# Kernel optimization log

Hardware: AMD Instinct MI355X
Metric: run time of the kernel (lower is better)

The kernel has to match this reference:

```python
import jax, jax.numpy as jnp
import numpy as np

B, S, P, D, H = 2, 4096, 1024, 1024, 16  # batch, byte seq, patches, d_model, heads


def setup_inputs() -> dict:
    key = jax.random.key(0)
    ks = jax.random.split(key, 8)
    init = 0.02
    queries = jax.random.normal(ks[0], (B, S, D), dtype=jnp.float32)
    patch_representations = jax.random.normal(ks[1], (B, P, D), dtype=jnp.float32)
    patch_boundaries = jax.random.randint(ks[2], (B, S), 0, 2, dtype=jnp.int32)
    wq = jax.random.normal(ks[3], (D, D), dtype=jnp.float32) * init
    wk = jax.random.normal(ks[4], (D, D), dtype=jnp.float32) * init
    wv = jax.random.normal(ks[5], (D, D), dtype=jnp.float32) * init
    wo = jax.random.normal(ks[6], (D, D), dtype=jnp.float32) * init
    bq = jnp.zeros((D,), jnp.float32)
    bk = jnp.zeros((D,), jnp.float32)
    bv = jnp.zeros((D,), jnp.float32)
    bo = jnp.zeros((D,), jnp.float32)
    return {"queries": queries, "patch_representations": patch_representations,
            "patch_boundaries": patch_boundaries,
            "wq": wq, "wk": wk, "wv": wv, "wo": wo,
            "bq": bq, "bk": bk, "bv": bv, "bo": bo}


def reference(queries, patch_representations, patch_boundaries,
              wq, wk, wv, wo, bq, bk, bv, bo):
    b, s, d = queries.shape
    p = patch_representations.shape[1]
    h = H
    dh = d // h
    scale = 1.0 / jnp.sqrt(jnp.asarray(dh, queries.dtype))

    # in-projections (torch Linear: x @ W.T + b)
    q = (queries @ wq.T + bq).reshape(b, s, h, dh)
    k = (patch_representations @ wk.T + bk).reshape(b, p, h, dh)
    v = (patch_representations @ wv.T + bv).reshape(b, p, h, dh)

    # scores: [b, h, s, p]
    scores = jnp.einsum('bqhd,bkhd->bhqk', q, k) * scale

    # data-dependent patch-boundary mask: byte t may attend to patch j iff j <= cumsum(boundaries)[t]
    patch_idx = jnp.cumsum(patch_boundaries, axis=1)          # [b, s]
    mask = jnp.arange(p)[None, None, :] > patch_idx[:, :, None]  # [b, s, p], True = masked
    scores = jnp.where(mask[:, None, :, :], jnp.finfo(scores.dtype).min, scores)

    attn = jax.nn.softmax(scores, axis=-1)                    # dropout inactive (eval)
    out = jnp.einsum('bhqk,bkhd->bqhd', attn, v).reshape(b, s, d)
    return out @ wo.T + bo
```

## Files before the change

### kernel.cpp

```cpp
#include <hip/hip_runtime.h>


#define B_ 2
#define S_ 4096
#define P_ 1024
#define D_ 1024
#define H_ 16
#define DH_ 64

#define NCONV 14336

typedef __attribute__((ext_vector_type(8))) short short8;
typedef __attribute__((ext_vector_type(4))) float f32x4;

#define KSCALE 0.18033688011112042f

#if __has_builtin(__builtin_amdgcn_exp2f)
#define EXP2(x) __builtin_amdgcn_exp2f(x)
#else
#define EXP2(x) exp2f(x)
#endif

static __device__ __forceinline__ unsigned short f2bf(float f) {
    unsigned int u = __float_as_uint(f);
    u += 0x7FFFu + ((u >> 16) & 1u);
    return (unsigned short)(u >> 16);
}

static __device__ __forceinline__ void gll16(const unsigned short* g,
                                             const unsigned short* l) {
    __builtin_amdgcn_global_load_lds(
        (const __attribute__((address_space(1))) unsigned int*)g,
        (__attribute__((address_space(3))) unsigned int*)l,
        16, 0, 0);
}

__global__ __launch_bounds__(256) void xattn_convert_all(
    const float* __restrict__ queries, const float* __restrict__ patches,
    const float* __restrict__ wq, const float* __restrict__ wk,
    const float* __restrict__ wv, const float* __restrict__ wo,
    unsigned short* __restrict__ qb, unsigned short* __restrict__ pb,
    unsigned short* __restrict__ wqb, unsigned short* __restrict__ wkb,
    unsigned short* __restrict__ wvb, unsigned short* __restrict__ wob,
    const int* __restrict__ bounds, int* __restrict__ pidx) {
    if (blockIdx.x >= NCONV) {
        __shared__ int sdata[256];
        int b = blockIdx.x - NCONV;
        int t = threadIdx.x;
        const int* src = bounds + b * S_ + t * 16;
        int vals[16];
        int run = 0;
#pragma unroll
        for (int i = 0; i < 16; ++i) { run += src[i]; vals[i] = run; }
        sdata[t] = run;
        __syncthreads();
        for (int off = 1; off < 256; off <<= 1) {
            int v = (t >= off) ? sdata[t - off] : 0;
            __syncthreads();
            sdata[t] += v;
            __syncthreads();
        }
        int prefix = (t > 0) ? sdata[t - 1] : 0;
        int* dst = pidx + b * S_ + t * 16;
#pragma unroll
        for (int i = 0; i < 16; ++i) dst[i] = prefix + vals[i];
        return;
    }
    const int NQ = (B_ * S_ * D_) / 4;
    const int NP = (B_ * P_ * D_) / 4;
    const int NW = (D_ * D_) / 4;
    int i = blockIdx.x * 256 + threadIdx.x;
    const float* src;
    unsigned short* dst;
    int j;
    if (i < NQ) { src = queries; dst = qb; j = i; }
    else if (i < NQ + NP) { src = patches; dst = pb; j = i - NQ; }
    else {
        int k = i - NQ - NP;
        int wsel = k >> 18;
        j = k & (NW - 1);
        if (wsel == 0) { src = wq; dst = wqb; }
        else if (wsel == 1) { src = wk; dst = wkb; }
        else if (wsel == 2) { src = wv; dst = wvb; }
        else { src = wo; dst = wob; }
    }
    float4 v = ((const float4*)src)[j];
    ushort4 o;
    o.x = f2bf(v.x); o.y = f2bf(v.y); o.z = f2bf(v.z); o.w = f2bf(v.w);
    ((ushort4*)dst)[j] = o;
}

__global__ __launch_bounds__(256) void xattn_gemm_qkv(
    const unsigned short* __restrict__ qb, const unsigned short* __restrict__ pb,
    const unsigned short* __restrict__ wqb, const unsigned short* __restrict__ wkb,
    const unsigned short* __restrict__ wvb,
    const float* __restrict__ bq, const float* __restrict__ bk,
    const float* __restrict__ bv,
    unsigned short* __restrict__ Qout, unsigned short* __restrict__ Kout,
    unsigned short* __restrict__ Vout) {
    const int K = 1024, N = 1024;
    const int byy = blockIdx.y;
    int z, my;
    if (byy < 64)      { z = 0; my = byy; }
    else if (byy < 80) { z = 1; my = byy - 64; }
    else               { z = 2; my = byy - 80; }
    const unsigned short* A = (z == 0) ? qb : pb;
    const unsigned short* W = (z == 0) ? wqb : ((z == 1) ? wkb : wvb);
    const float* bias = (z == 0) ? bq : ((z == 1) ? bk : bv);

    __shared__ unsigned short As[2][128 * 32];
    __shared__ unsigned short Bs[2][128 * 32];

    const int m0 = my * 128;
    const int n0 = blockIdx.x * 128;
    const int t = threadIdx.x;
    const int w = t >> 6;
    const int l = t & 63;
    const int fr = l & 15, fq = l >> 4;
    const int wr = w >> 1, wc = w & 1;

    const int r0s = t >> 2;
    const int csw = ((t & 3) ^ ((t >> 3) & 3)) * 8;
    const unsigned short* Ap0 = A + (size_t)(m0 + r0s) * K + csw;
    const unsigned short* Ap1 = A + (size_t)(m0 + 64 + r0s) * K + csw;
    const unsigned short* Wp0 = W + (size_t)(n0 + r0s) * K + csw;
    const unsigned short* Wp1 = W + (size_t)(n0 + 64 + r0s) * K + csw;

    const int gsw = (fq ^ ((fr >> 1) & 3)) * 8;

    f32x4 acc[4][4];
#pragma unroll
    for (int i = 0; i < 4; ++i)
#pragma unroll
        for (int j = 0; j < 4; ++j) acc[i][j] = (f32x4){0.f, 0.f, 0.f, 0.f};

    gll16(Ap0, &As[0][w * 512]);
    gll16(Ap1, &As[0][2048 + w * 512]);
    gll16(Wp0, &Bs[0][w * 512]);
    gll16(Wp1, &Bs[0][2048 + w * 512]);

    for (int kt = 0; kt < 32; ++kt) {
        __builtin_amdgcn_s_barrier();
        if (kt + 1 < 32) {
            const int nb = (kt + 1) & 1;
            const int ks = (kt + 1) * 32;
            gll16(Ap0 + ks, &As[nb][w * 512]);
            gll16(Ap1 + ks, &As[nb][2048 + w * 512]);
            gll16(Wp0 + ks, &Bs[nb][w * 512]);
            gll16(Wp1 + ks, &Bs[nb][2048 + w * 512]);
            asm volatile("s_waitcnt vmcnt(4)" ::: "memory");
        } else {
            asm volatile("s_waitcnt vmcnt(0)" ::: "memory");
        }
        __builtin_amdgcn_sched_barrier(0);
        __builtin_amdgcn_s_barrier();

        const unsigned short* Ac = As[kt & 1];
        const unsigned short* Bc = Bs[kt & 1];
        short8 af[4], bf[4];
#pragma unroll
        for (int i = 0; i < 4; ++i)
            af[i] = *(const short8*)&Ac[(wr * 64 + i * 16 + fr) * 32 + gsw];
#pragma unroll
        for (int j = 0; j < 4; ++j)
            bf[j] = *(const short8*)&Bc[(wc * 64 + j * 16 + fr) * 32 + gsw];
        __builtin_amdgcn_s_setprio(1);
#pragma unroll
        for (int i = 0; i < 4; ++i)
#pragma unroll
            for (int j = 0; j < 4; ++j)
                acc[i][j] = __builtin_amdgcn_mfma_f32_16x16x32_bf16(af[i], bf[j], acc[i][j], 0, 0, 0);
        __builtin_amdgcn_s_setprio(0);
    }

#pragma unroll
    for (int j = 0; j < 4; ++j) {
        int n = n0 + wc * 64 + j * 16 + fr;
        float bvv = bias[n];
#pragma unroll
        for (int i = 0; i < 4; ++i) {
            int mbase = m0 + wr * 64 + i * 16 + fq * 4;
#pragma unroll
            for (int r = 0; r < 4; ++r) {
                float val = acc[i][j][r] + bvv;
                int m = mbase + r;
                if (z == 0) {
                    Qout[(size_t)m * N + n] = f2bf(val * KSCALE);
                } else if (z == 1) {
                    Kout[(size_t)m * N + n] = f2bf(val);
                } else {
                    int bb = m >> 10, c = m & (P_ - 1);
                    int hh = n >> 6, d = n & 63;
                    int cl = c & 63;
                    int cp = (c & 960) | (((cl & 15) << 2) | (cl >> 4));
                    Vout[(((size_t)(bb * H_ + hh)) * 64 + d) * P_ + cp] = f2bf(val);
                }
            }
        }
    }
}

__global__ __launch_bounds__(256) void xattn_gemm_o(
    const unsigned short* __restrict__ A,
    const unsigned short* __restrict__ W,
    const float* __restrict__ bias,
    float* __restrict__ Cout) {
    const int K = 1024, N = 1024;
    __shared__ unsigned short As[2][128 * 32];
    __shared__ unsigned short Bs[2][128 * 32];

    const int m0 = blockIdx.y * 128;
    const int n0 = blockIdx.x * 128;
    const int t = threadIdx.x;
    const int w = t >> 6;
    const int l = t & 63;
    const int fr = l & 15, fq = l >> 4;
    const int wr = w >> 1, wc = w & 1;

    const int r0s = t >> 2;
    const int csw = ((t & 3) ^ ((t >> 3) & 3)) * 8;
    const unsigned short* Ap0 = A + (size_t)(m0 + r0s) * K + csw;
    const unsigned short* Ap1 = A + (size_t)(m0 + 64 + r0s) * K + csw;
    const unsigned short* Wp0 = W + (size_t)(n0 + r0s) * K + csw;
    const unsigned short* Wp1 = W + (size_t)(n0 + 64 + r0s) * K + csw;

    const int gsw = (fq ^ ((fr >> 1) & 3)) * 8;

    f32x4 acc[4][4];
#pragma unroll
    for (int i = 0; i < 4; ++i)
#pragma unroll
        for (int j = 0; j < 4; ++j) acc[i][j] = (f32x4){0.f, 0.f, 0.f, 0.f};

    gll16(Ap0, &As[0][w * 512]);
    gll16(Ap1, &As[0][2048 + w * 512]);
    gll16(Wp0, &Bs[0][w * 512]);
    gll16(Wp1, &Bs[0][2048 + w * 512]);

    for (int kt = 0; kt < 32; ++kt) {
        __builtin_amdgcn_s_barrier();
        if (kt + 1 < 32) {
            const int nb = (kt + 1) & 1;
            const int ks = (kt + 1) * 32;
            gll16(Ap0 + ks, &As[nb][w * 512]);
            gll16(Ap1 + ks, &As[nb][2048 + w * 512]);
            gll16(Wp0 + ks, &Bs[nb][w * 512]);
            gll16(Wp1 + ks, &Bs[nb][2048 + w * 512]);
            asm volatile("s_waitcnt vmcnt(4)" ::: "memory");
        } else {
            asm volatile("s_waitcnt vmcnt(0)" ::: "memory");
        }
        __builtin_amdgcn_sched_barrier(0);
        __builtin_amdgcn_s_barrier();

        const unsigned short* Ac = As[kt & 1];
        const unsigned short* Bc = Bs[kt & 1];
        short8 af[4], bf[4];
#pragma unroll
        for (int i = 0; i < 4; ++i)
            af[i] = *(const short8*)&Ac[(wr * 64 + i * 16 + fr) * 32 + gsw];
#pragma unroll
        for (int j = 0; j < 4; ++j)
            bf[j] = *(const short8*)&Bc[(wc * 64 + j * 16 + fr) * 32 + gsw];
        __builtin_amdgcn_s_setprio(1);
#pragma unroll
        for (int i = 0; i < 4; ++i)
#pragma unroll
            for (int j = 0; j < 4; ++j)
                acc[i][j] = __builtin_amdgcn_mfma_f32_16x16x32_bf16(af[i], bf[j], acc[i][j], 0, 0, 0);
        __builtin_amdgcn_s_setprio(0);
    }

#pragma unroll
    for (int j = 0; j < 4; ++j) {
        int n = n0 + wc * 64 + j * 16 + fr;
        float bvv = bias[n];
#pragma unroll
        for (int i = 0; i < 4; ++i) {
            int mbase = m0 + wr * 64 + i * 16 + fq * 4;
#pragma unroll
            for (int r = 0; r < 4; ++r)
                Cout[(size_t)(mbase + r) * N + n] = acc[i][j][r] + bvv;
        }
    }
}

__global__ __launch_bounds__(256) void xattn_attn_mfma(
    const unsigned short* __restrict__ Qb,
    const unsigned short* __restrict__ Kb,
    const unsigned short* __restrict__ Vtb,
    const int* __restrict__ pidx,
    unsigned short* __restrict__ Ob) {
    __shared__ unsigned short Ks[2][64 * 64];
    __shared__ unsigned short Vs[2][64 * 64];
    __shared__ unsigned short Ps[64 * 64];

    const int q0 = (63 - blockIdx.x) * 64;
    const int h = blockIdx.y;
    const int b = blockIdx.z;
    const int t = threadIdx.x;
    const int w = t >> 6, l = t & 63;
    const int fr = l & 15, fq = l >> 4;

    const unsigned short* qrow =
        Qb + (size_t)(b * S_ + q0 + w * 16 + fr) * D_ + h * DH_ + fq * 8;
    short8 qf0 = *(const short8*)qrow;
    short8 qf1 = *(const short8*)(qrow + 32);

    int prow[4];
#pragma unroll
    for (int r = 0; r < 4; ++r)
        prow[r] = pidx[b * S_ + q0 + w * 16 + fq * 4 + r];
    const int limit = pidx[b * S_ + q0 + 63];
    const int ntiles = (min(limit, P_ - 1) + 64) >> 6;
    const int nfull = (pidx[b * S_ + q0] + 1) >> 6;

    float lsum[4] = {0.f, 0.f, 0.f, 0.f};
    f32x4 oacc[4];
#pragma unroll
    for (int nt = 0; nt < 4; ++nt) oacc[nt] = (f32x4){0.f, 0.f, 0.f, 0.f};

    const int srow = l >> 3;
    const int g = (l & 7) ^ srow;
    const unsigned short* kbase = Kb + (size_t)(b * P_) * D_ + h * DH_;
    const unsigned short* vbase = Vtb + (size_t)(b * H_ + h) * 64 * P_;
    const unsigned short* kp0 = kbase + (size_t)(w * 16 + srow) * D_ + g * 8;
    const unsigned short* kp1 = kp0 + (size_t)8 * D_;
    const unsigned short* vp0 = vbase + (size_t)(w * 16 + srow) * P_ + g * 8;
    const unsigned short* vp1 = vp0 + (size_t)8 * P_;

    gll16(kp0, &Ks[0][w * 1024]);
    gll16(kp1, &Ks[0][w * 1024 + 512]);
    gll16(vp0, &Vs[0][w * 1024]);
    gll16(vp1, &Vs[0][w * 1024 + 512]);
    kp0 += (size_t)64 * D_; kp1 += (size_t)64 * D_;
    vp0 += 64; vp1 += 64;

    const int sw = (fq ^ (fr & 7)) * 8;
    int cur = 0;

    for (int kt = 0; kt < ntiles; ++kt) {
        __builtin_amdgcn_s_barrier();
        if (kt + 1 < ntiles) {
            const int nb = cur ^ 1;
            gll16(kp0, &Ks[nb][w * 1024]);
            gll16(kp1, &Ks[nb][w * 1024 + 512]);
            gll16(vp0, &Vs[nb][w * 1024]);
            gll16(vp1, &Vs[nb][w * 1024 + 512]);
            kp0 += (size_t)64 * D_; kp1 += (size_t)64 * D_;
            vp0 += 64; vp1 += 64;
            asm volatile("s_waitcnt vmcnt(4)" ::: "memory");
        } else {
            asm volatile("s_waitcnt vmcnt(0)" ::: "memory");
        }
        __builtin_amdgcn_sched_barrier(0);
        __builtin_amdgcn_s_barrier();

        const unsigned short* Kc = Ks[cur];
        const unsigned short* Vc = Vs[cur];
        const int c0 = kt * 64;
        const int maskme = (kt >= nfull);

        f32x4 s[4];
        __builtin_amdgcn_s_setprio(1);
#pragma unroll
        for (int nt = 0; nt < 4; ++nt) {
            short8 kf0 = *(const short8*)&Kc[(nt * 16 + fr) * 64 + sw];
            short8 kf1 = *(const short8*)&Kc[(nt * 16 + fr) * 64 + (sw ^ 32)];
            f32x4 a = (f32x4){0.f, 0.f, 0.f, 0.f};
            a = __builtin_amdgcn_mfma_f32_16x16x32_bf16(qf0, kf0, a, 0, 0, 0);
            a = __builtin_amdgcn_mfma_f32_16x16x32_bf16(qf1, kf1, a, 0, 0, 0);
            s[nt] = a;
        }
        __builtin_amdgcn_s_setprio(0);

        if (maskme) {
#pragma unroll
            for (int nt = 0; nt < 4; ++nt) {
                const int col = c0 + nt * 16 + fr;
#pragma unroll
                for (int r = 0; r < 4; ++r) {
                    float p = EXP2(s[nt][r]);
                    p = (col > prow[r]) ? 0.f : p;
                    s[nt][r] = p;
                    lsum[r] += p;
                }
            }
        } else {
#pragma unroll
            for (int nt = 0; nt < 4; ++nt) {
#pragma unroll
                for (int r = 0; r < 4; ++r) {
                    float p = EXP2(s[nt][r]);
                    s[nt][r] = p;
                    lsum[r] += p;
                }
            }
        }

#pragma unroll
        for (int r = 0; r < 4; ++r) {
            uint2 pk;
            pk.x = __builtin_amdgcn_perm(__float_as_uint(s[1][r]),
                                         __float_as_uint(s[0][r]), 0x07060302u);
            pk.y = __builtin_amdgcn_perm(__float_as_uint(s[3][r]),
                                         __float_as_uint(s[2][r]), 0x07060302u);
            const int pr = w * 16 + fq * 4 + r;
            const int pg = (((fr >> 1) ^ (pr & 7)) << 3) | ((fr & 1) << 2);
            *(uint2*)&Ps[pr * 64 + pg] = pk;
        }

        const int prr = (w * 16 + fr) * 64;
        short8 pf0 = *(const short8*)&Ps[prr + sw];
        short8 pf1 = *(const short8*)&Ps[prr + (sw ^ 32)];
        __builtin_amdgcn_s_setprio(1);
#pragma unroll
        for (int nt = 0; nt < 4; ++nt) {
            short8 vf0 = *(const short8*)&Vc[(nt * 16 + fr) * 64 + sw];
            short8 vf1 = *(const short8*)&Vc[(nt * 16 + fr) * 64 + (sw ^ 32)];
            oacc[nt] = __builtin_amdgcn_mfma_f32_16x16x32_bf16(pf0, vf0, oacc[nt], 0, 0, 0);
            oacc[nt] = __builtin_amdgcn_mfma_f32_16x16x32_bf16(pf1, vf1, oacc[nt], 0, 0, 0);
        }
        __builtin_amdgcn_s_setprio(0);

        cur ^= 1;
    }

#pragma unroll
    for (int off = 1; off < 16; off <<= 1) {
#pragma unroll
        for (int r = 0; r < 4; ++r)
            lsum[r] += __shfl_xor(lsum[r], off);
    }
    float inv[4];
#pragma unroll
    for (int r = 0; r < 4; ++r) inv[r] = 1.0f / lsum[r];

    unsigned short* obase = Ob + (size_t)(b * S_ + q0 + w * 16) * D_ + h * DH_;
#pragma unroll
    for (int nt = 0; nt < 4; ++nt)
#pragma unroll
        for (int r = 0; r < 4; ++r)
            obase[(size_t)(fq * 4 + r) * D_ + nt * 16 + fr] =
                f2bf(oacc[nt][r] * inv[r]);
}

extern "C" void kernel_launch(void* const* d_in, const int* in_sizes, int n_in,
                              void* d_out, int out_size, void* d_ws, size_t ws_size,
                              hipStream_t stream) {
    const float* queries = (const float*)d_in[0];
    const float* patches = (const float*)d_in[1];
    const int* bounds    = (const int*)d_in[2];
    const float* wq = (const float*)d_in[3];
    const float* wk = (const float*)d_in[4];
    const float* wv = (const float*)d_in[5];
    const float* wo = (const float*)d_in[6];
    const float* bq = (const float*)d_in[7];
    const float* bk = (const float*)d_in[8];
    const float* bv = (const float*)d_in[9];
    const float* bo = (const float*)d_in[10];
    float* out = (float*)d_out;

    char* ws = (char*)d_ws;
    unsigned short* qb    = (unsigned short*)(ws + 0);
    unsigned short* pb    = (unsigned short*)(ws + 16777216);
    unsigned short* wqb   = (unsigned short*)(ws + 20971520);
    unsigned short* wkb   = (unsigned short*)(ws + 23068672);
    unsigned short* wvb   = (unsigned short*)(ws + 25165824);
    unsigned short* wob   = (unsigned short*)(ws + 27262976);
    unsigned short* Qbf   = (unsigned short*)(ws + 29360128);
    unsigned short* Kbf   = (unsigned short*)(ws + 46137344);
    unsigned short* Vtb   = (unsigned short*)(ws + 50331648);
    unsigned short* attnb = (unsigned short*)(ws + 54525952);
    int* pidx             = (int*)(ws + 71303168);

    xattn_convert_all<<<dim3(NCONV + B_), 256, 0, stream>>>(
        queries, patches, wq, wk, wv, wo, qb, pb, wqb, wkb, wvb, wob,
        bounds, pidx);
    xattn_gemm_qkv<<<dim3(8, 96), 256, 0, stream>>>(
        qb, pb, wqb, wkb, wvb, bq, bk, bv, Qbf, Kbf, Vtb);
    xattn_attn_mfma<<<dim3(S_ / 64, H_, B_), 256, 0, stream>>>(
        Qbf, Kbf, Vtb, pidx, attnb);
    xattn_gemm_o<<<dim3(8, 64), 256, 0, stream>>>(attnb, wob, bo, out);
}
```

Before: 235.7 us.

## Switch attention to 32x32x16 MFMA with fragment-ordered K/V and register-only P

Rewrites the attention kernel to use 32x32x16 bf16 MFMA, with 128 queries per block and 32 per wave. The QKV GEMM now writes K and V in a pre-swizzled fragment layout so each tile is loaded with contiguous gll16 copies and read straight from LDS without extra indexing. The P matrix is converted with v_cvt_pk_bf16_f32 and reshuffled across lanes with v_permlane32_swap, so it no longer round-trips through LDS. The cost is half as many attention blocks and new gfx950-specific instructions.

```diff
diff --git a/kernel.cpp b/kernel.cpp
--- a/kernel.cpp
+++ b/kernel.cpp
@@ -12,6 +12,7 @@
 
 typedef __attribute__((ext_vector_type(8))) short short8;
 typedef __attribute__((ext_vector_type(4))) float f32x4;
+typedef __attribute__((ext_vector_type(16))) float f32x16;
 
 #define KSCALE 0.18033688011112042f
 
@@ -25,6 +26,16 @@
     unsigned int u = __float_as_uint(f);
     u += 0x7FFFu + ((u >> 16) & 1u);
     return (unsigned short)(u >> 16);
+}
+
+static __device__ __forceinline__ unsigned int cvtpk(float lo, float hi) {
+    unsigned int r;
+    asm("v_cvt_pk_bf16_f32 %0, %1, %2" : "=v"(r) : "v"(lo), "v"(hi));
+    return r;
+}
+
+static __device__ __forceinline__ void plswap(unsigned int& x, unsigned int& y) {
+    asm volatile("v_permlane32_swap_b32 %0, %1" : "+v"(x), "+v"(y));
 }
 
 static __device__ __forceinline__ void gll16(const unsigned short* g,
@@ -187,13 +198,19 @@
                 if (z == 0) {
                     Qout[(size_t)m * N + n] = f2bf(val * KSCALE);
                 } else if (z == 1) {
-                    Kout[(size_t)m * N + n] = f2bf(val);
+                    int bb = m >> 10, p = m & (P_ - 1);
+                    int hh = n >> 6, k = n & 63;
+                    size_t base = ((size_t)((bb * H_ + hh) * 16 + (p >> 6))) * 4096;
+                    int off = (((p >> 5) & 1) * 4 + (k >> 4)) * 512 +
+                              (((k >> 3) & 1) * 32 + (p & 31)) * 8 + (k & 7);
+                    Kout[base + off] = f2bf(val);
                 } else {
-                    int bb = m >> 10, c = m & (P_ - 1);
+                    int bb = m >> 10, p = m & (P_ - 1);
                     int hh = n >> 6, d = n & 63;
-                    int cl = c & 63;
-                    int cp = (c & 960) | (((cl & 15) << 2) | (cl >> 4));
-                    Vout[(((size_t)(bb * H_ + hh)) * 64 + d) * P_ + cp] = f2bf(val);
+                    size_t base = ((size_t)((bb * H_ + hh) * 16 + (p >> 6))) * 4096;
+                    int off = ((d >> 5) * 4 + ((p >> 4) & 3)) * 512 +
+                              ((((p >> 3) & 1) * 32) + (d & 31)) * 8 + (p & 7);
+                    Vout[base + off] = f2bf(val);
                 }
             }
         }
@@ -287,68 +304,55 @@
 
 __global__ __launch_bounds__(256) void xattn_attn_mfma(
     const unsigned short* __restrict__ Qb,
-    const unsigned short* __restrict__ Kb,
-    const unsigned short* __restrict__ Vtb,
+    const unsigned short* __restrict__ Kf,
+    const unsigned short* __restrict__ Vf,
     const int* __restrict__ pidx,
     unsigned short* __restrict__ Ob) {
-    __shared__ unsigned short Ks[2][64 * 64];
-    __shared__ unsigned short Vs[2][64 * 64];
-    __shared__ unsigned short Ps[64 * 64];
-
-    const int q0 = (63 - blockIdx.x) * 64;
+    __shared__ unsigned short Ks[2][4096];
+    __shared__ unsigned short Vs[2][4096];
+
+    const int q0 = (31 - blockIdx.x) * 128;
     const int h = blockIdx.y;
     const int b = blockIdx.z;
     const int t = threadIdx.x;
     const int w = t >> 6, l = t & 63;
-    const int fr = l & 15, fq = l >> 4;
+    const int lq = l & 31, lh = l >> 5;
+    const int qw = q0 + w * 32;
 
     const unsigned short* qrow =
-        Qb + (size_t)(b * S_ + q0 + w * 16 + fr) * D_ + h * DH_ + fq * 8;
-    short8 qf0 = *(const short8*)qrow;
-    short8 qf1 = *(const short8*)(qrow + 32);
-
-    int prow[4];
-#pragma unroll
-    for (int r = 0; r < 4; ++r)
-        prow[r] = pidx[b * S_ + q0 + w * 16 + fq * 4 + r];
-    const int limit = pidx[b * S_ + q0 + 63];
+        Qb + (size_t)(b * S_ + qw + lq) * D_ + h * DH_ + lh * 8;
+    short8 qf[4];
+#pragma unroll
+    for (int ks = 0; ks < 4; ++ks) qf[ks] = *(const short8*)(qrow + ks * 16);
+
+    const int prow = pidx[b * S_ + qw + lq];
+    const int limit = pidx[b * S_ + q0 + 127];
     const int ntiles = (min(limit, P_ - 1) + 64) >> 6;
     const int nfull = (pidx[b * S_ + q0] + 1) >> 6;
 
-    float lsum[4] = {0.f, 0.f, 0.f, 0.f};
-    f32x4 oacc[4];
-#pragma unroll
-    for (int nt = 0; nt < 4; ++nt) oacc[nt] = (f32x4){0.f, 0.f, 0.f, 0.f};
-
-    const int srow = l >> 3;
-    const int g = (l & 7) ^ srow;
-    const unsigned short* kbase = Kb + (size_t)(b * P_) * D_ + h * DH_;
-    const unsigned short* vbase = Vtb + (size_t)(b * H_ + h) * 64 * P_;
-    const unsigned short* kp0 = kbase + (size_t)(w * 16 + srow) * D_ + g * 8;
-    const unsigned short* kp1 = kp0 + (size_t)8 * D_;
-    const unsigned short* vp0 = vbase + (size_t)(w * 16 + srow) * P_ + g * 8;
-    const unsigned short* vp1 = vp0 + (size_t)8 * P_;
-
-    gll16(kp0, &Ks[0][w * 1024]);
-    gll16(kp1, &Ks[0][w * 1024 + 512]);
-    gll16(vp0, &Vs[0][w * 1024]);
-    gll16(vp1, &Vs[0][w * 1024 + 512]);
-    kp0 += (size_t)64 * D_; kp1 += (size_t)64 * D_;
-    vp0 += 64; vp1 += 64;
-
-    const int sw = (fq ^ (fr & 7)) * 8;
-    int cur = 0;
+    float l4[4] = {0.f, 0.f, 0.f, 0.f};
+    f32x16 oacc[2] = {{}, {}};
+
+    const unsigned short* kfb =
+        Kf + (size_t)((b * H_ + h) * 16) * 4096 + (2 * w) * 512 + l * 8;
+    const unsigned short* vfb =
+        Vf + (size_t)((b * H_ + h) * 16) * 4096 + (2 * w) * 512 + l * 8;
+
+    gll16(kfb, &Ks[0][(2 * w) * 512]);
+    gll16(kfb + 512, &Ks[0][(2 * w + 1) * 512]);
+    gll16(vfb, &Vs[0][(2 * w) * 512]);
+    gll16(vfb + 512, &Vs[0][(2 * w + 1) * 512]);
 
     for (int kt = 0; kt < ntiles; ++kt) {
         __builtin_amdgcn_s_barrier();
         if (kt + 1 < ntiles) {
-            const int nb = cur ^ 1;
-            gll16(kp0, &Ks[nb][w * 1024]);
-            gll16(kp1, &Ks[nb][w * 1024 + 512]);
-            gll16(vp0, &Vs[nb][w * 1024]);
-            gll16(vp1, &Vs[nb][w * 1024 + 512]);
-            kp0 += (size_t)64 * D_; kp1 += (size_t)64 * D_;
-            vp0 += 64; vp1 += 64;
+            const int nb = (kt + 1) & 1;
+            const unsigned short* kn = kfb + (size_t)(kt + 1) * 4096;
+            const unsigned short* vn = vfb + (size_t)(kt + 1) * 4096;
+            gll16(kn, &Ks[nb][(2 * w) * 512]);
+            gll16(kn + 512, &Ks[nb][(2 * w + 1) * 512]);
+            gll16(vn, &Vs[nb][(2 * w) * 512]);
+            gll16(vn + 512, &Vs[nb][(2 * w + 1) * 512]);
             asm volatile("s_waitcnt vmcnt(4)" ::: "memory");
         } else {
             asm volatile("s_waitcnt vmcnt(0)" ::: "memory");
@@ -356,93 +360,84 @@
         __builtin_amdgcn_sched_barrier(0);
         __builtin_amdgcn_s_barrier();
 
-        const unsigned short* Kc = Ks[cur];
-        const unsigned short* Vc = Vs[cur];
+        const unsigned short* Kc = Ks[kt & 1];
+        const unsigned short* Vc = Vs[kt & 1];
         const int c0 = kt * 64;
-        const int maskme = (kt >= nfull);
-
-        f32x4 s[4];
+
+        f32x16 sa[2];
         __builtin_amdgcn_s_setprio(1);
 #pragma unroll
-        for (int nt = 0; nt < 4; ++nt) {
-            short8 kf0 = *(const short8*)&Kc[(nt * 16 + fr) * 64 + sw];
-            short8 kf1 = *(const short8*)&Kc[(nt * 16 + fr) * 64 + (sw ^ 32)];
-            f32x4 a = (f32x4){0.f, 0.f, 0.f, 0.f};
-            a = __builtin_amdgcn_mfma_f32_16x16x32_bf16(qf0, kf0, a, 0, 0, 0);
-            a = __builtin_amdgcn_mfma_f32_16x16x32_bf16(qf1, kf1, a, 0, 0, 0);
-            s[nt] = a;
+        for (int at = 0; at < 2; ++at) {
+            f32x16 a = {};
+#pragma unroll
+            for (int ks = 0; ks < 4; ++ks) {
+                short8 kfr = *(const short8*)&Kc[(at * 4 + ks) * 512 + l * 8];
+                a = __builtin_amdgcn_mfma_f32_32x32x16_bf16(kfr, qf[ks], a, 0, 0, 0);
+            }
+            sa[at] = a;
         }
         __builtin_amdgcn_s_setprio(0);
 
-        if (maskme) {
-#pragma unroll
-            for (int nt = 0; nt < 4; ++nt) {
-                const int col = c0 + nt * 16 + fr;
-#pragma unroll
-                for (int r = 0; r < 4; ++r) {
-                    float p = EXP2(s[nt][r]);
-                    p = (col > prow[r]) ? 0.f : p;
-                    s[nt][r] = p;
-                    lsum[r] += p;
+        if (kt >= nfull) {
+#pragma unroll
+            for (int at = 0; at < 2; ++at)
+#pragma unroll
+                for (int r = 0; r < 16; ++r) {
+                    const int pg = c0 + at * 32 + (r & 3) + 8 * (r >> 2) + 4 * lh;
+                    float p = EXP2(sa[at][r]);
+                    p = (pg > prow) ? 0.f : p;
+                    sa[at][r] = p;
+                    l4[r & 3] += p;
                 }
+        } else {
+#pragma unroll
+            for (int at = 0; at < 2; ++at)
+#pragma unroll
+                for (int r = 0; r < 16; ++r) {
+                    float p = EXP2(sa[at][r]);
+                    sa[at][r] = p;
+                    l4[r & 3] += p;
+                }
+        }
+
+        short8 pa[4];
+#pragma unroll
+        for (int ps = 0; ps < 4; ++ps) {
+            const int pt = ps >> 1;
+            const int rA = (ps & 1) * 8;
+            unsigned int X0 = cvtpk(sa[pt][rA + 0], sa[pt][rA + 1]);
+            unsigned int Y0 = cvtpk(sa[pt][rA + 4], sa[pt][rA + 5]);
+            unsigned int X1 = cvtpk(sa[pt][rA + 2], sa[pt][rA + 3]);
+            unsigned int Y1 = cvtpk(sa[pt][rA + 6], sa[pt][rA + 7]);
+            plswap(X0, Y0);
+            plswap(X1, Y1);
+            uint4 u = {X0, X1, Y0, Y1};
+            pa[ps] = *(short8*)&u;
+        }
+
+        __builtin_amdgcn_s_setprio(1);
+#pragma unroll
+        for (int dt = 0; dt < 2; ++dt)
+#pragma unroll
+            for (int ps = 0; ps < 4; ++ps) {
+                short8 vfr = *(const short8*)&Vc[(dt * 4 + ps) * 512 + l * 8];
+                oacc[dt] = __builtin_amdgcn_mfma_f32_32x32x16_bf16(pa[ps], vfr, oacc[dt], 0, 0, 0);
             }
-        } else {
-#pragma unroll
-            for (int nt = 0; nt < 4; ++nt) {
-#pragma unroll
-                for (int r = 0; r < 4; ++r) {
-                    float p = EXP2(s[nt][r]);
-                    s[nt][r] = p;
-                    lsum[r] += p;
-                }
-            }
-        }
-
-#pragma unroll
-        for (int r = 0; r < 4; ++r) {
-            uint2 pk;
-            pk.x = __builtin_amdgcn_perm(__float_as_uint(s[1][r]),
-                                         __float_as_uint(s[0][r]), 0x07060302u);
-            pk.y = __builtin_amdgcn_perm(__float_as_uint(s[3][r]),
-                                         __float_as_uint(s[2][r]), 0x07060302u);
-            const int pr = w * 16 + fq * 4 + r;
-            const int pg = (((fr >> 1) ^ (pr & 7)) << 3) | ((fr & 1) << 2);
-            *(uint2*)&Ps[pr * 64 + pg] = pk;
-        }
-
-        const int prr = (w * 16 + fr) * 64;
-        short8 pf0 = *(const short8*)&Ps[prr + sw];
-        short8 pf1 = *(const short8*)&Ps[prr + (sw ^ 32)];
-        __builtin_amdgcn_s_setprio(1);
-#pragma unroll
-        for (int nt = 0; nt < 4; ++nt) {
-            short8 vf0 = *(const short8*)&Vc[(nt * 16 + fr) * 64 + sw];
-            short8 vf1 = *(const short8*)&Vc[(nt * 16 + fr) * 64 + (sw ^ 32)];
-            oacc[nt] = __builtin_amdgcn_mfma_f32_16x16x32_bf16(pf0, vf0, oacc[nt], 0, 0, 0);
-            oacc[nt] = __builtin_amdgcn_mfma_f32_16x16x32_bf16(pf1, vf1, oacc[nt], 0, 0, 0);
-        }
         __builtin_amdgcn_s_setprio(0);
-
-        cur ^= 1;
-    }
-
-#pragma unroll
-    for (int off = 1; off < 16; off <<= 1) {
-#pragma unroll
-        for (int r = 0; r < 4; ++r)
-            lsum[r] += __shfl_xor(lsum[r], off);
-    }
-    float inv[4];
-#pragma unroll
-    for (int r = 0; r < 4; ++r) inv[r] = 1.0f / lsum[r];
-
-    unsigned short* obase = Ob + (size_t)(b * S_ + q0 + w * 16) * D_ + h * DH_;
-#pragma unroll
-    for (int nt = 0; nt < 4; ++nt)
-#pragma unroll
-        for (int r = 0; r < 4; ++r)
-            obase[(size_t)(fq * 4 + r) * D_ + nt * 16 + fr] =
-                f2bf(oacc[nt][r] * inv[r]);
+    }
+
+    float lsum = (l4[0] + l4[1]) + (l4[2] + l4[3]);
+    lsum += __shfl_xor(lsum, 32);
+    const float inv = 1.0f / lsum;
+
+    unsigned short* ob = Ob + (size_t)(b * S_ + qw) * D_ + h * DH_;
+#pragma unroll
+    for (int r = 0; r < 16; ++r) {
+        const int qr = (r & 3) + 8 * (r >> 2) + 4 * lh;
+        const float invr = __shfl(inv, qr);
+        ob[(size_t)qr * D_ + lq] = f2bf(oacc[0][r] * invr);
+        ob[(size_t)qr * D_ + 32 + lq] = f2bf(oacc[1][r] * invr);
+    }
 }
 
 extern "C" void kernel_launch(void* const* d_in, const int* in_sizes, int n_in,
@@ -469,8 +464,8 @@
     unsigned short* wvb   = (unsigned short*)(ws + 25165824);
     unsigned short* wob   = (unsigned short*)(ws + 27262976);
     unsigned short* Qbf   = (unsigned short*)(ws + 29360128);
-    unsigned short* Kbf   = (unsigned short*)(ws + 46137344);
-    unsigned short* Vtb   = (unsigned short*)(ws + 50331648);
+    unsigned short* Kfr   = (unsigned short*)(ws + 46137344);
+    unsigned short* Vfr   = (unsigned short*)(ws + 50331648);
     unsigned short* attnb = (unsigned short*)(ws + 54525952);
     int* pidx             = (int*)(ws + 71303168);
 
@@ -478,8 +473,8 @@
         queries, patches, wq, wk, wv, wo, qb, pb, wqb, wkb, wvb, wob,
         bounds, pidx);
     xattn_gemm_qkv<<<dim3(8, 96), 256, 0, stream>>>(
-        qb, pb, wqb, wkb, wvb, bq, bk, bv, Qbf, Kbf, Vtb);
-    xattn_attn_mfma<<<dim3(S_ / 64, H_, B_), 256, 0, stream>>>(
-        Qbf, Kbf, Vtb, pidx, attnb);
+        qb, pb, wqb, wkb, wvb, bq, bk, bv, Qbf, Kfr, Vfr);
+    xattn_attn_mfma<<<dim3(S_ / 128, H_, B_), 256, 0, stream>>>(
+        Qbf, Kfr, Vfr, pidx, attnb);
     xattn_gemm_o<<<dim3(8, 64), 256, 0, stream>>>(attnb, wob, bo, out);
 }
```

Result: no change. 233.3 us (-1.0%).
